# Performance work log

Measured on AMD Instinct MI355X. Metric: run time of the kernel, lower is better.

## Reference

```python
import jax, jax.numpy as jnp
import numpy as np

N, E, H, B, G, C = 50000, 800000, 64, 3, 256, 250
EPS = 1e-5
NEG_SLOPE = 0.2


def _bn(x, g, b):
    # BatchNorm1d, training-mode batch statistics (biased variance)
    m = x.mean(0)
    v = x.var(0)
    return g * (x - m) * jax.lax.rsqrt(v + EPS) + b


def _prelu(x, a):
    return jnp.where(x >= 0, x, a * x)


def _gatv2(x, src, dst, edge_attr, Wl, bl, Wr, br, We, att, bias):
    # PyG GATv2Conv, heads=1, aggr='sum':
    #   x_j = lin_l(x[src]), x_i = lin_r(x[dst]), e = lin_edge(edge_attr)
    #   alpha = softmax_dst(att . leaky_relu(x_j + x_i + e))
    #   out[i] = sum_j alpha_ij * x_j + bias
    xl = x @ Wl.T + bl            # [N,H]
    xr = x @ Wr.T + br            # [N,H]
    ee = edge_attr @ We.T         # [E,H]
    m = xl[src] + xr[dst] + ee    # [E,H]
    logits = jax.nn.leaky_relu(m, NEG_SLOPE) @ att  # [E]
    mx = jax.ops.segment_max(logits, dst, num_segments=N)
    ex = jnp.exp(logits - mx[dst])
    denom = jax.ops.segment_sum(ex, dst, num_segments=N)
    alpha = ex / denom[dst]
    out = jax.ops.segment_sum(alpha[:, None] * xl[src], dst, num_segments=N)
    return out + bias


def setup_inputs() -> dict:
    key = jax.random.key(0)
    ks = iter(jax.random.split(key, 40))
    s = 0.1
    inp = {
        "x": jax.random.normal(next(ks), (N, 64), jnp.float32),
        "edge_index": jax.random.randint(next(ks), (2, E), 0, N),
        "edge_attr": jax.random.normal(next(ks), (E, 2), jnp.float32),
        "batch": jnp.sort(jax.random.randint(next(ks), (N,), 0, G)),
        # pre layer
        "pre_W": jax.random.normal(next(ks), (H, 64), jnp.float32) * s,
        "pre_b": jnp.zeros((H,), jnp.float32),
        "pre_g": jnp.ones((H,), jnp.float32),
        "pre_beta": jnp.zeros((H,), jnp.float32),
        "pre_a": jnp.float32(0.25),
        # blocks: [B, 2(conv1/conv2), ...]
        "blk_Wl": jax.random.normal(next(ks), (B, 2, H, H), jnp.float32) * s,
        "blk_bl": jnp.zeros((B, 2, H), jnp.float32),
        "blk_Wr": jax.random.normal(next(ks), (B, 2, H, H), jnp.float32) * s,
        "blk_br": jnp.zeros((B, 2, H), jnp.float32),
        "blk_We": jax.random.normal(next(ks), (B, 2, H, 2), jnp.float32) * s,
        "blk_att": jax.random.normal(next(ks), (B, 2, H), jnp.float32) * s,
        "blk_cb": jnp.zeros((B, 2, H), jnp.float32),
        "blk_bng": jnp.ones((B, 2, H), jnp.float32),
        "blk_bnb": jnp.zeros((B, 2, H), jnp.float32),
        "blk_pa": jnp.full((B, 2), 0.25, jnp.float32),
        # post layers
        "post_W1": jax.random.normal(next(ks), (4 * H, H), jnp.float32) * s,
        "post_b1": jnp.zeros((4 * H,), jnp.float32),
        "post_g": jnp.ones((4 * H,), jnp.float32),
        "post_beta": jnp.zeros((4 * H,), jnp.float32),
        "post_a": jnp.float32(0.25),
        "post_W2": jax.random.normal(next(ks), (C, 4 * H), jnp.float32) * s,
        "post_b2": jnp.zeros((C,), jnp.float32),
    }
    return inp


def reference(x, edge_index, edge_attr, batch, pre_W, pre_b, pre_g, pre_beta,
              pre_a, blk_Wl, blk_bl, blk_Wr, blk_br, blk_We, blk_att, blk_cb,
              blk_bng, blk_bnb, blk_pa, post_W1, post_b1, post_g, post_beta,
              post_a, post_W2, post_b2):
    src, dst = edge_index[0], edge_index[1]
    h = _prelu(_bn(x @ pre_W.T + pre_b, pre_g, pre_beta), pre_a)
    for i in range(B):
        res = h
        h = _gatv2(h, src, dst, edge_attr, blk_Wl[i, 0], blk_bl[i, 0],
                   blk_Wr[i, 0], blk_br[i, 0], blk_We[i, 0], blk_att[i, 0],
                   blk_cb[i, 0])
        h = _prelu(_bn(h, blk_bng[i, 0], blk_bnb[i, 0]), blk_pa[i, 0])
        h = _gatv2(h, src, dst, edge_attr, blk_Wl[i, 1], blk_bl[i, 1],
                   blk_Wr[i, 1], blk_br[i, 1], blk_We[i, 1], blk_att[i, 1],
                   blk_cb[i, 1])
        h = _bn(h, blk_bng[i, 1], blk_bnb[i, 1])
        h = _prelu(res + h, blk_pa[i, 1])
    pooled = jax.ops.segment_max(h, batch, num_segments=G)  # [G,H]
    z = _prelu(_bn(pooled @ post_W1.T + post_b1, post_g, post_beta), post_a)
    return z @ post_W2.T + post_b2
```

## Files before the change

### kernel.cpp

```cpp
#include <hip/hip_runtime.h>

static constexpr int kN = 50000;
static constexpr int kE = 800000;
static constexpr int kH = 64;
static constexpr int kG = 256;
static constexpr int kC = 250;
static constexpr int kNH = kN * kH;
static constexpr float kEps = 1e-5f;
static constexpr float kNeg = 0.2f;
static constexpr float kNegInf = -3.402823466e38f;
static constexpr int kScanB = (kN + 1023) / 1024;

__device__ float g_F0[kNH];
__device__ float g_F1[kNH];
__device__ float g_XL[kNH];
__device__ float g_XR[kNH];
__device__ float g_ACC[kNH];
__device__ int g_DEG[kN];
__device__ int g_CUR[kN];
__device__ int g_ROW[kN + 1];
__device__ int g_BTOT[64];
__device__ int g_BOFF[64];
__device__ int g_CSRC[kE];
__device__ float2 g_CEA[kE];
__device__ float g_SUMS2[7 * 128];
__device__ unsigned g_POOL[kG * kH];
__device__ float g_Z[kG * 256];
__device__ float g_HSUMS[512];

__device__ inline unsigned fenc(float f) {
  unsigned u = __float_as_uint(f);
  return (u & 0x80000000u) ? ~u : (u | 0x80000000u);
}
__device__ inline float fdec(unsigned u) {
  return (u & 0x80000000u) ? __uint_as_float(u & 0x7FFFFFFFu)
                           : __uint_as_float(~u);
}

__global__ void GCN_41781441855659_kernel() {
  int i = blockIdx.x * 256 + threadIdx.x;
  int stride = gridDim.x * 256;
  for (int k = i; k < kN; k += stride) {
    g_DEG[k] = 0;
    g_CUR[k] = 0;
  }
  for (int k = i; k < kG * kH; k += stride) g_POOL[k] = 0u;
  for (int k = i; k < 7 * 128; k += stride) g_SUMS2[k] = 0.0f;
  for (int k = i; k < 512; k += stride) g_HSUMS[k] = 0.0f;
}

__global__ void k_deg_count(const int* dst) {
  int e = blockIdx.x * 256 + threadIdx.x;
  if (e < kE) atomicAdd(&g_DEG[dst[e]], 1);
}

__global__ void k_scan1() {
  __shared__ int s[1024];
  int b = blockIdx.x, tid = threadIdx.x;
  int idx = b * 1024 + tid;
  int v = (idx < kN) ? g_DEG[idx] : 0;
  s[tid] = v;
  __syncthreads();
  for (int off = 1; off < 1024; off <<= 1) {
    int t = (tid >= off) ? s[tid - off] : 0;
    __syncthreads();
    s[tid] += t;
    __syncthreads();
  }
  if (idx < kN) g_ROW[idx] = s[tid] - v;
  if (tid == 1023) g_BTOT[b] = s[1023];
}

__global__ void k_scan2() {
  if (threadIdx.x == 0) {
    int run = 0;
    for (int b = 0; b < kScanB; b++) {
      g_BOFF[b] = run;
      run += g_BTOT[b];
    }
    g_ROW[kN] = run;
  }
}

__global__ void k_scan3() {
  int b = blockIdx.x;
  int idx = b * 1024 + threadIdx.x;
  if (idx < kN) g_ROW[idx] += g_BOFF[b];
}

__global__ void k_csr_scatter(const int* src, const int* dst,
                              const float* ea) {
  int e = blockIdx.x * 256 + threadIdx.x;
  if (e >= kE) return;
  int d = dst[e];
  int slot = g_ROW[d] + atomicAdd(&g_CUR[d], 1);
  g_CSRC[slot] = src[e];
  g_CEA[slot] = make_float2(ea[e * 2 + 0], ea[e * 2 + 1]);
}

__global__ void k_gemm_dual(int sel, const float* Xext, const float* Wl,
                            const float* bl, const float* Wr,
                            const float* br) {
  const float* X = (sel == 0) ? Xext : (sel == 1 ? g_F0 : g_F1);
  __shared__ float wl[64][64];
  __shared__ float wr[64][64];
  for (int i = threadIdx.x; i < 4096; i += 256) {
    int c = i >> 6, k = i & 63;
    wl[k][c] = Wl[i];
    wr[k][c] = Wr[i];
  }
  __syncthreads();
  int lane = threadIdx.x & 63;
  int w = threadIdx.x >> 6;
  int r0 = blockIdx.x * 64;
  for (int rl = w; rl < 64; rl += 4) {
    int r = r0 + rl;
    if (r >= kN) break;
    const float* xrow = X + (size_t)r * kH;
    float accl = bl[lane];
    float accr = br[lane];
#pragma unroll
    for (int k = 0; k < 64; k++) {
      float xv = xrow[k];
      accl += xv * wl[k][lane];
      accr += xv * wr[k][lane];
    }
    g_XL[(size_t)r * 64 + lane] = accl;
    g_XR[(size_t)r * 64 + lane] = accr;
  }
}

__global__ void k_gat_fused(const float* We, const float* att) {
  int wid = threadIdx.x >> 6;
  int d = blockIdx.x * 4 + wid;
  if (d >= kN) return;
  int lane = threadIdx.x & 63;
  int grp = lane >> 4;
  int q = lane & 15;
  int c0 = q * 4;
  int beg = g_ROW[d], end = g_ROW[d + 1];
  float4 outv = make_float4(0.0f, 0.0f, 0.0f, 0.0f);
  if (beg < end) {
    const float4 xr = *(const float4*)&g_XR[(size_t)d * 64 + c0];
    const float4 wea = *(const float4*)&We[c0 * 2];
    const float4 web = *(const float4*)&We[c0 * 2 + 4];
    const float4 at4 = *(const float4*)&att[c0];
    float m = kNegInf, den = 0.0f;
    float4 acc = make_float4(0.0f, 0.0f, 0.0f, 0.0f);
    for (int i = beg + grp; i < end; i += 4) {
      int s = g_CSRC[i];
      float2 eav = g_CEA[i];
      const float4 xl = *(const float4*)&g_XL[(size_t)s * 64 + c0];
      float me0 = xl.x + xr.x + eav.x * wea.x + eav.y * wea.y;
      float me1 = xl.y + xr.y + eav.x * wea.z + eav.y * wea.w;
      float me2 = xl.z + xr.z + eav.x * web.x + eav.y * web.y;
      float me3 = xl.w + xr.w + eav.x * web.z + eav.y * web.w;
      me0 = (me0 >= 0.0f) ? me0 : kNeg * me0;
      me1 = (me1 >= 0.0f) ? me1 : kNeg * me1;
      me2 = (me2 >= 0.0f) ? me2 : kNeg * me2;
      me3 = (me3 >= 0.0f) ? me3 : kNeg * me3;
      float part =
          me0 * at4.x + me1 * at4.y + me2 * at4.z + me3 * at4.w;
      part += __shfl_xor(part, 1);
      part += __shfl_xor(part, 2);
      part += __shfl_xor(part, 4);
      part += __shfl_xor(part, 8);
      if (part <= m) {
        float w = __expf(part - m);
        den += w;
        acc.x += w * xl.x;
        acc.y += w * xl.y;
        acc.z += w * xl.z;
        acc.w += w * xl.w;
      } else {
        float sc = __expf(m - part);
        den = den * sc + 1.0f;
        acc.x = acc.x * sc + xl.x;
        acc.y = acc.y * sc + xl.y;
        acc.z = acc.z * sc + xl.z;
        acc.w = acc.w * sc + xl.w;
        m = part;
      }
    }
#pragma unroll
    for (int off = 16; off <= 32; off <<= 1) {
      float mo = __shfl_xor(m, off);
      float deno = __shfl_xor(den, off);
      float ax = __shfl_xor(acc.x, off);
      float ay = __shfl_xor(acc.y, off);
      float az = __shfl_xor(acc.z, off);
      float aw = __shfl_xor(acc.w, off);
      float mn = fmaxf(m, mo);
      float sa = __expf(m - mn);
      float sb = __expf(mo - mn);
      den = den * sa + deno * sb;
      acc.x = acc.x * sa + ax * sb;
      acc.y = acc.y * sa + ay * sb;
      acc.z = acc.z * sa + az * sb;
      acc.w = acc.w * sa + aw * sb;
      m = mn;
    }
    float inv = 1.0f / den;
    outv = make_float4(acc.x * inv, acc.y * inv, acc.z * inv, acc.w * inv);
  }
  if (grp == 0) *(float4*)&g_ACC[(size_t)d * 64 + c0] = outv;
}

__global__ void k_bn_stats(int layer, int sel) {
  const float* x = (sel == 1) ? g_XL : g_ACC;
  float* SUMS = g_SUMS2 + layer * 128;
  int c = threadIdx.x & 63;
  int sub = threadIdx.x >> 6;
  float s = 0.0f, ss = 0.0f;
  for (int r = blockIdx.x * 4 + sub; r < kN; r += gridDim.x * 4) {
    float v = x[(size_t)r * 64 + c];
    s += v;
    ss += v * v;
  }
  __shared__ float ls[4][64];
  __shared__ float lss[4][64];
  ls[sub][c] = s;
  lss[sub][c] = ss;
  __syncthreads();
  if (threadIdx.x < 64) {
    float t = ls[0][c] + ls[1][c] + ls[2][c] + ls[3][c];
    float tt = lss[0][c] + lss[1][c] + lss[2][c] + lss[3][c];
    atomicAdd(&SUMS[c], t);
    atomicAdd(&SUMS[64 + c], tt);
  }
}

__global__ void k_bn_apply(int layer, int sel_in, int use_res, int sel_out,
                           const float* g, const float* beta,
                           const float* pa) {
  const float* x = (sel_in == 1) ? g_XL : g_ACC;
  float* out = (sel_out == 1) ? g_F0 : g_F1;
  const float* SUMS = g_SUMS2 + layer * 128;
  const float inv = 1.0f / (float)kN;
  float a = pa[0];
  for (int idx = blockIdx.x * 256 + threadIdx.x; idx < kNH;
       idx += gridDim.x * 256) {
    int c = idx & 63;
    float mean = SUMS[c] * inv;
    float var = SUMS[64 + c] * inv - mean * mean;
    float sc = g[c] * rsqrtf(var + kEps);
    float sh = beta[c] - mean * sc;
    float v = x[idx] * sc + sh;
    if (use_res) v += g_F0[idx];
    out[idx] = (v >= 0.0f) ? v : a * v;
  }
}

__global__ void k_pool_max(const int* batch) {
  int r = blockIdx.x * 4 + (threadIdx.x >> 6);
  int lane = threadIdx.x & 63;
  if (r >= kN) return;
  int g = batch[r];
  float v = g_F0[(size_t)r * 64 + lane];
  atomicMax(&g_POOL[g * 64 + lane], fenc(v));
}

__global__ void k_head_gemm1(const float* W1, const float* b1) {
  int g = blockIdx.x;
  int j = threadIdx.x;
  __shared__ float p[64];
  if (j < 64) p[j] = fdec(g_POOL[g * 64 + j]);
  __syncthreads();
  float y = b1[j];
  const float* wrow = W1 + (size_t)j * 64;
#pragma unroll
  for (int k = 0; k < 64; k++) y += p[k] * wrow[k];
  g_Z[(size_t)g * 256 + j] = y;
  atomicAdd(&g_HSUMS[j], y);
  atomicAdd(&g_HSUMS[256 + j], y * y);
}

__global__ void k_head_out(const float* g1, const float* beta1,
                           const float* pa, const float* W2, const float* b2,
                           float* out) {
  int g = blockIdx.x;
  int j = threadIdx.x;
  __shared__ float zs[256];
  {
    const float inv = 1.0f / (float)kG;
    float mean = g_HSUMS[j] * inv;
    float var = g_HSUMS[256 + j] * inv - mean * mean;
    float sc = g1[j] * rsqrtf(var + kEps);
    float a = pa[0];
    float z = (g_Z[(size_t)g * 256 + j] - mean) * sc + beta1[j];
    zs[j] = (z >= 0.0f) ? z : a * z;
  }
  __syncthreads();
  if (j < kC) {
    const float* wrow = W2 + (size_t)j * 256;
    float acc = b2[j];
#pragma unroll 8
    for (int k = 0; k < 256; k++) acc += zs[k] * wrow[k];
    out[(size_t)g * kC + j] = acc;
  }
}

extern "C" void kernel_launch(void* const* d_in, const int* in_sizes, int n_in,
                              void* d_out, int out_size, void* d_ws,
                              size_t ws_size, hipStream_t stream) {
  const float* x = (const float*)d_in[0];
  const int* ei = (const int*)d_in[1];
  const int* src = ei;
  const int* dst = ei + kE;
  const float* ea = (const float*)d_in[2];
  const int* batch = (const int*)d_in[3];
  const float* pre_W = (const float*)d_in[4];
  const float* pre_b = (const float*)d_in[5];
  const float* pre_g = (const float*)d_in[6];
  const float* pre_beta = (const float*)d_in[7];
  const float* pre_a = (const float*)d_in[8];
  const float* blk_Wl = (const float*)d_in[9];
  const float* blk_bl = (const float*)d_in[10];
  const float* blk_Wr = (const float*)d_in[11];
  const float* blk_br = (const float*)d_in[12];
  const float* blk_We = (const float*)d_in[13];
  const float* blk_att = (const float*)d_in[14];
  const float* blk_bng = (const float*)d_in[16];
  const float* blk_bnb = (const float*)d_in[17];
  const float* blk_pa = (const float*)d_in[18];
  const float* post_W1 = (const float*)d_in[19];
  const float* post_b1 = (const float*)d_in[20];
  const float* post_g = (const float*)d_in[21];
  const float* post_beta = (const float*)d_in[22];
  const float* post_a = (const float*)d_in[23];
  const float* post_W2 = (const float*)d_in[24];
  const float* post_b2 = (const float*)d_in[25];

  const int gGemm = (kN + 63) / 64;
  const int gEdge = (kE + 255) / 256;
  const int gNode4 = (kN + 3) / 4;

  GCN_41781441855659_kernel<<<256, 256, 0, stream>>>();
  k_deg_count<<<gEdge, 256, 0, stream>>>(dst);
  k_scan1<<<kScanB, 1024, 0, stream>>>();
  k_scan2<<<1, 64, 0, stream>>>();
  k_scan3<<<kScanB, 1024, 0, stream>>>();
  k_csr_scatter<<<gEdge, 256, 0, stream>>>(src, dst, ea);

  k_gemm_dual<<<gGemm, 256, 0, stream>>>(0, x, pre_W, pre_b, pre_W, pre_b);
  k_bn_stats<<<256, 256, 0, stream>>>(0, 1);
  k_bn_apply<<<2048, 256, 0, stream>>>(0, 1, 0, 1, pre_g, pre_beta, pre_a);

  for (int l = 0; l < 6; l++) {
    int j = l & 1;
    const float* Wl = blk_Wl + (size_t)l * kH * kH;
    const float* bl = blk_bl + (size_t)l * kH;
    const float* Wr = blk_Wr + (size_t)l * kH * kH;
    const float* br = blk_br + (size_t)l * kH;
    const float* We = blk_We + (size_t)l * kH * 2;
    const float* att = blk_att + (size_t)l * kH;
    const float* bng = blk_bng + (size_t)l * kH;
    const float* bnb = blk_bnb + (size_t)l * kH;
    const float* pa = blk_pa + l;

    k_gemm_dual<<<gGemm, 256, 0, stream>>>((j == 0) ? 1 : 2, x, Wl, bl, Wr,
                                           br);
    k_gat_fused<<<gNode4, 256, 0, stream>>>(We, att);
    k_bn_stats<<<256, 256, 0, stream>>>(1 + l, 2);
    if (j == 0) {
      k_bn_apply<<<2048, 256, 0, stream>>>(1 + l, 2, 0, 2, bng, bnb, pa);
    } else {
      k_bn_apply<<<2048, 256, 0, stream>>>(1 + l, 2, 1, 1, bng, bnb, pa);
    }
  }

  k_pool_max<<<gNode4, 256, 0, stream>>>(batch);
  k_head_gemm1<<<kG, 256, 0, stream>>>(post_W1, post_b1);
  k_head_out<<<kG, 256, 0, stream>>>(post_g, post_beta, post_a, post_W2,
                                     post_b2, (float*)d_out);
}
```

Before: 1.065 ms.

## Register-tile dual GEMM, widen GAT lanes to 8 channels, split CSR scatter

```diff
diff --git a/kernel.cpp b/kernel.cpp
--- a/kernel.cpp
+++ b/kernel.cpp
@@ -21,6 +21,7 @@
 __device__ int g_ROW[kN + 1];
 __device__ int g_BTOT[64];
 __device__ int g_BOFF[64];
+__device__ int g_PERM[kE];
 __device__ int g_CSRC[kE];
 __device__ float2 g_CEA[kE];
 __device__ float g_SUMS2[7 * 128];
@@ -88,45 +89,85 @@
   if (idx < kN) g_ROW[idx] += g_BOFF[b];
 }
 
-__global__ void k_csr_scatter(const int* src, const int* dst,
-                              const float* ea) {
+__global__ void k_csr_scatter(const int* dst) {
   int e = blockIdx.x * 256 + threadIdx.x;
   if (e >= kE) return;
   int d = dst[e];
   int slot = g_ROW[d] + atomicAdd(&g_CUR[d], 1);
-  g_CSRC[slot] = src[e];
-  g_CEA[slot] = make_float2(ea[e * 2 + 0], ea[e * 2 + 1]);
+  g_PERM[slot] = e;
+}
+
+__global__ void k_csr_reorder(const int* src, const float* ea) {
+  int i = blockIdx.x * 256 + threadIdx.x;
+  if (i >= kE) return;
+  int e = g_PERM[i];
+  g_CSRC[i] = src[e];
+  g_CEA[i] = make_float2(ea[e * 2 + 0], ea[e * 2 + 1]);
 }
 
 __global__ void k_gemm_dual(int sel, const float* Xext, const float* Wl,
                             const float* bl, const float* Wr,
                             const float* br) {
   const float* X = (sel == 0) ? Xext : (sel == 1 ? g_F0 : g_F1);
-  __shared__ float wl[64][64];
-  __shared__ float wr[64][64];
+  __shared__ float wl[64][68];
+  __shared__ float wr[64][68];
+  __shared__ float xs[64][68];
   for (int i = threadIdx.x; i < 4096; i += 256) {
     int c = i >> 6, k = i & 63;
     wl[k][c] = Wl[i];
     wr[k][c] = Wr[i];
   }
+  int r0 = blockIdx.x * 64;
+  for (int i = threadIdx.x; i < 4096; i += 256) {
+    int r = i >> 6, k = i & 63;
+    int rr = r0 + r;
+    xs[r][k] = (rr < kN) ? X[(size_t)rr * 64 + k] : 0.0f;
+  }
   __syncthreads();
-  int lane = threadIdx.x & 63;
-  int w = threadIdx.x >> 6;
-  int r0 = blockIdx.x * 64;
-  for (int rl = w; rl < 64; rl += 4) {
-    int r = r0 + rl;
-    if (r >= kN) break;
-    const float* xrow = X + (size_t)r * kH;
-    float accl = bl[lane];
-    float accr = br[lane];
-#pragma unroll
-    for (int k = 0; k < 64; k++) {
-      float xv = xrow[k];
-      accl += xv * wl[k][lane];
-      accr += xv * wr[k][lane];
-    }
-    g_XL[(size_t)r * 64 + lane] = accl;
-    g_XR[(size_t)r * 64 + lane] = accr;
+  int q = threadIdx.x & 15;
+  int rs = threadIdx.x >> 4;
+  int c0 = q * 4;
+  float4 bl4 = *(const float4*)&bl[c0];
+  float4 br4 = *(const float4*)&br[c0];
+  float4 al[4], ar[4];
+#pragma unroll
+  for (int t = 0; t < 4; t++) {
+    al[t] = bl4;
+    ar[t] = br4;
+  }
+  for (int k4 = 0; k4 < 64; k4 += 4) {
+    float4 xq[4];
+#pragma unroll
+    for (int t = 0; t < 4; t++)
+      xq[t] = *(const float4*)&xs[rs + t * 16][k4];
+#pragma unroll
+    for (int kk = 0; kk < 4; kk++) {
+      float4 wl4 = *(const float4*)&wl[k4 + kk][c0];
+      float4 wr4 = *(const float4*)&wr[k4 + kk][c0];
+#pragma unroll
+      for (int t = 0; t < 4; t++) {
+        float xv = (kk == 0) ? xq[t].x
+                 : (kk == 1) ? xq[t].y
+                 : (kk == 2) ? xq[t].z
+                             : xq[t].w;
+        al[t].x += xv * wl4.x;
+        al[t].y += xv * wl4.y;
+        al[t].z += xv * wl4.z;
+        al[t].w += xv * wl4.w;
+        ar[t].x += xv * wr4.x;
+        ar[t].y += xv * wr4.y;
+        ar[t].z += xv * wr4.z;
+        ar[t].w += xv * wr4.w;
+      }
+    }
+  }
+#pragma unroll
+  for (int t = 0; t < 4; t++) {
+    int r = r0 + rs + t * 16;
+    if (r < kN) {
+      *(float4*)&g_XL[(size_t)r * 64 + c0] = al[t];
+      *(float4*)&g_XR[(size_t)r * 64 + c0] = ar[t];
+    }
   }
 }
 
@@ -135,75 +176,93 @@
   int d = blockIdx.x * 4 + wid;
   if (d >= kN) return;
   int lane = threadIdx.x & 63;
-  int grp = lane >> 4;
-  int q = lane & 15;
-  int c0 = q * 4;
+  int grp = lane >> 3;
+  int h = lane & 7;
+  int c0 = h * 8;
   int beg = g_ROW[d], end = g_ROW[d + 1];
-  float4 outv = make_float4(0.0f, 0.0f, 0.0f, 0.0f);
+  float4 o0 = make_float4(0.f, 0.f, 0.f, 0.f);
+  float4 o1 = make_float4(0.f, 0.f, 0.f, 0.f);
   if (beg < end) {
-    const float4 xr = *(const float4*)&g_XR[(size_t)d * 64 + c0];
-    const float4 wea = *(const float4*)&We[c0 * 2];
-    const float4 web = *(const float4*)&We[c0 * 2 + 4];
-    const float4 at4 = *(const float4*)&att[c0];
+    const float4 xr0 = *(const float4*)&g_XR[(size_t)d * 64 + c0];
+    const float4 xr1 = *(const float4*)&g_XR[(size_t)d * 64 + c0 + 4];
+    const float4 we0 = *(const float4*)&We[c0 * 2];
+    const float4 we1 = *(const float4*)&We[c0 * 2 + 4];
+    const float4 we2 = *(const float4*)&We[c0 * 2 + 8];
+    const float4 we3 = *(const float4*)&We[c0 * 2 + 12];
+    const float4 at0 = *(const float4*)&att[c0];
+    const float4 at1 = *(const float4*)&att[c0 + 4];
     float m = kNegInf, den = 0.0f;
-    float4 acc = make_float4(0.0f, 0.0f, 0.0f, 0.0f);
-    for (int i = beg + grp; i < end; i += 4) {
+    float4 a0 = make_float4(0.f, 0.f, 0.f, 0.f);
+    float4 a1 = make_float4(0.f, 0.f, 0.f, 0.f);
+    for (int i = beg + grp; i < end; i += 8) {
       int s = g_CSRC[i];
       float2 eav = g_CEA[i];
-      const float4 xl = *(const float4*)&g_XL[(size_t)s * 64 + c0];
-      float me0 = xl.x + xr.x + eav.x * wea.x + eav.y * wea.y;
-      float me1 = xl.y + xr.y + eav.x * wea.z + eav.y * wea.w;
-      float me2 = xl.z + xr.z + eav.x * web.x + eav.y * web.y;
-      float me3 = xl.w + xr.w + eav.x * web.z + eav.y * web.w;
-      me0 = (me0 >= 0.0f) ? me0 : kNeg * me0;
-      me1 = (me1 >= 0.0f) ? me1 : kNeg * me1;
-      me2 = (me2 >= 0.0f) ? me2 : kNeg * me2;
-      me3 = (me3 >= 0.0f) ? me3 : kNeg * me3;
-      float part =
-          me0 * at4.x + me1 * at4.y + me2 * at4.z + me3 * at4.w;
+      const float4 xl0 = *(const float4*)&g_XL[(size_t)s * 64 + c0];
+      const float4 xl1 = *(const float4*)&g_XL[(size_t)s * 64 + c0 + 4];
+      float m0 = xl0.x + xr0.x + eav.x * we0.x + eav.y * we0.y;
+      float m1 = xl0.y + xr0.y + eav.x * we0.z + eav.y * we0.w;
+      float m2 = xl0.z + xr0.z + eav.x * we1.x + eav.y * we1.y;
+      float m3 = xl0.w + xr0.w + eav.x * we1.z + eav.y * we1.w;
+      float m4 = xl1.x + xr1.x + eav.x * we2.x + eav.y * we2.y;
+      float m5 = xl1.y + xr1.y + eav.x * we2.z + eav.y * we2.w;
+      float m6 = xl1.z + xr1.z + eav.x * we3.x + eav.y * we3.y;
+      float m7 = xl1.w + xr1.w + eav.x * we3.z + eav.y * we3.w;
+      m0 = (m0 >= 0.f) ? m0 : kNeg * m0;
+      m1 = (m1 >= 0.f) ? m1 : kNeg * m1;
+      m2 = (m2 >= 0.f) ? m2 : kNeg * m2;
+      m3 = (m3 >= 0.f) ? m3 : kNeg * m3;
+      m4 = (m4 >= 0.f) ? m4 : kNeg * m4;
+      m5 = (m5 >= 0.f) ? m5 : kNeg * m5;
+      m6 = (m6 >= 0.f) ? m6 : kNeg * m6;
+      m7 = (m7 >= 0.f) ? m7 : kNeg * m7;
+      float part = m0 * at0.x + m1 * at0.y + m2 * at0.z + m3 * at0.w +
+                   m4 * at1.x + m5 * at1.y + m6 * at1.z + m7 * at1.w;
       part += __shfl_xor(part, 1);
       part += __shfl_xor(part, 2);
       part += __shfl_xor(part, 4);
-      part += __shfl_xor(part, 8);
       if (part <= m) {
         float w = __expf(part - m);
         den += w;
-        acc.x += w * xl.x;
-        acc.y += w * xl.y;
-        acc.z += w * xl.z;
-        acc.w += w * xl.w;
+        a0.x += w * xl0.x; a0.y += w * xl0.y;
+        a0.z += w * xl0.z; a0.w += w * xl0.w;
+        a1.x += w * xl1.x; a1.y += w * xl1.y;
+        a1.z += w * xl1.z; a1.w += w * xl1.w;
       } else {
         float sc = __expf(m - part);
         den = den * sc + 1.0f;
-        acc.x = acc.x * sc + xl.x;
-        acc.y = acc.y * sc + xl.y;
-        acc.z = acc.z * sc + xl.z;
-        acc.w = acc.w * sc + xl.w;
+        a0.x = a0.x * sc + xl0.x; a0.y = a0.y * sc + xl0.y;
+        a0.z = a0.z * sc + xl0.z; a0.w = a0.w * sc + xl0.w;
+        a1.x = a1.x * sc + xl1.x; a1.y = a1.y * sc + xl1.y;
+        a1.z = a1.z * sc + xl1.z; a1.w = a1.w * sc + xl1.w;
         m = part;
       }
     }
 #pragma unroll
-    for (int off = 16; off <= 32; off <<= 1) {
+    for (int off = 8; off <= 32; off <<= 1) {
       float mo = __shfl_xor(m, off);
       float deno = __shfl_xor(den, off);
-      float ax = __shfl_xor(acc.x, off);
-      float ay = __shfl_xor(acc.y, off);
-      float az = __shfl_xor(acc.z, off);
-      float aw = __shfl_xor(acc.w, off);
+      float b0x = __shfl_xor(a0.x, off), b0y = __shfl_xor(a0.y, off);
+      float b0z = __shfl_xor(a0.z, off), b0w = __shfl_xor(a0.w, off);
+      float b1x = __shfl_xor(a1.x, off), b1y = __shfl_xor(a1.y, off);
+      float b1z = __shfl_xor(a1.z, off), b1w = __shfl_xor(a1.w, off);
       float mn = fmaxf(m, mo);
       float sa = __expf(m - mn);
       float sb = __expf(mo - mn);
       den = den * sa + deno * sb;
-      acc.x = acc.x * sa + ax * sb;
-      acc.y = acc.y * sa + ay * sb;
-      acc.z = acc.z * sa + az * sb;
-      acc.w = acc.w * sa + aw * sb;
+      a0.x = a0.x * sa + b0x * sb; a0.y = a0.y * sa + b0y * sb;
+      a0.z = a0.z * sa + b0z * sb; a0.w = a0.w * sa + b0w * sb;
+      a1.x = a1.x * sa + b1x * sb; a1.y = a1.y * sa + b1y * sb;
+      a1.z = a1.z * sa + b1z * sb; a1.w = a1.w * sa + b1w * sb;
       m = mn;
     }
     float inv = 1.0f / den;
-    outv = make_float4(acc.x * inv, acc.y * inv, acc.z * inv, acc.w * inv);
-  }
-  if (grp == 0) *(float4*)&g_ACC[(size_t)d * 64 + c0] = outv;
+    o0 = make_float4(a0.x * inv, a0.y * inv, a0.z * inv, a0.w * inv);
+    o1 = make_float4(a1.x * inv, a1.y * inv, a1.z * inv, a1.w * inv);
+  }
+  if (grp == 0) {
+    *(float4*)&g_ACC[(size_t)d * 64 + c0] = o0;
+    *(float4*)&g_ACC[(size_t)d * 64 + c0 + 4] = o1;
+  }
 }
 
 __global__ void k_bn_stats(int layer, int sel) {
@@ -340,7 +399,8 @@
   k_scan1<<<kScanB, 1024, 0, stream>>>();
   k_scan2<<<1, 64, 0, stream>>>();
   k_scan3<<<kScanB, 1024, 0, stream>>>();
-  k_csr_scatter<<<gEdge, 256, 0, stream>>>(src, dst, ea);
+  k_csr_scatter<<<gEdge, 256, 0, stream>>>(dst);
+  k_csr_reorder<<<gEdge, 256, 0, stream>>>(src, ea);
 
   k_gemm_dual<<<gGemm, 256, 0, stream>>>(0, x, pre_W, pre_b, pre_W, pre_b);
   k_bn_stats<<<256, 256, 0, stream>>>(0, 1);
```

Result: slower. 1.791 ms (+68.3%).
